# Optimization experiments

Hardware: AMD Instinct MI355X
Metric: run time of the kernel (lower is better)

The kernel has to match this reference:

```python
import jax, jax.numpy as jnp
import numpy as np

NG, NQ, E, H, L, B = 500000, 100000, 1000000, 128, 4, 1024
EMB, GDIM, NTYPES = 16, 32, 31


def _xavier(key, shape):
    fan_in, fan_out = shape[-2], shape[-1]
    lim = float(np.sqrt(6.0 / (fan_in + fan_out)))
    return jax.random.uniform(key, shape, minval=-lim, maxval=lim, dtype=jnp.float32)


def setup_inputs():
    key = jax.random.key(0)
    ks = iter(jax.random.split(key, 64))
    nk = lambda: next(ks)
    inp = {}
    inp["gate_type_idx"] = jax.random.randint(nk(), (NG,), 0, NTYPES)
    inp["gate_arity"] = jax.random.randint(nk(), (NG,), 1, 3)
    inp["gate_is_directional"] = jax.random.randint(nk(), (NG,), 0, 2)
    inp["gate_index_norm"] = jax.random.uniform(nk(), (NG,), dtype=jnp.float32)
    inp["qubit_degree_norm"] = jax.random.uniform(nk(), (NQ,), dtype=jnp.float32)
    inp["src_g2q"] = jax.random.randint(nk(), (E,), 0, NG)
    inp["dst_g2q"] = jax.random.randint(nk(), (E,), 0, NQ)
    inp["src_q2g"] = jax.random.randint(nk(), (E,), 0, NQ)
    inp["dst_q2g"] = jax.random.randint(nk(), (E,), 0, NG)
    inp["gate_batch"] = jnp.sort(jax.random.randint(nk(), (NG,), 0, B))
    inp["qubit_batch"] = jnp.sort(jax.random.randint(nk(), (NQ,), 0, B))
    inp["global_features"] = jax.random.normal(nk(), (B, GDIM), dtype=jnp.float32)
    inp["backend_bit"] = jax.random.randint(nk(), (B,), 0, 2).astype(jnp.float32)
    inp["precision_bit"] = jax.random.randint(nk(), (B,), 0, 2).astype(jnp.float32)
    inp["emb_table"] = jax.random.normal(nk(), (NTYPES, EMB), dtype=jnp.float32) / np.sqrt(EMB).astype(np.float32)
    inp["gate_proj_W"] = _xavier(nk(), (EMB + 3, H)); inp["gate_proj_b"] = jnp.zeros((H,), jnp.float32)
    inp["qubit_proj_W"] = _xavier(nk(), (1, H)); inp["qubit_proj_b"] = jnp.zeros((H,), jnp.float32)
    inp["g2q_ll_W"] = _xavier(nk(), (L, H, H)); inp["g2q_ll_b"] = jnp.zeros((L, H), jnp.float32)
    inp["g2q_lr_W"] = _xavier(nk(), (L, H, H)); inp["g2q_lr_b"] = jnp.zeros((L, H), jnp.float32)
    inp["q2g_ll_W"] = _xavier(nk(), (L, H, H)); inp["q2g_ll_b"] = jnp.zeros((L, H), jnp.float32)
    inp["q2g_lr_W"] = _xavier(nk(), (L, H, H)); inp["q2g_lr_b"] = jnp.zeros((L, H), jnp.float32)
    inp["gate_ln_g"] = jnp.ones((L, H), jnp.float32); inp["gate_ln_b"] = jnp.zeros((L, H), jnp.float32)
    inp["qubit_ln_g"] = jnp.ones((L, H), jnp.float32); inp["qubit_ln_b"] = jnp.zeros((L, H), jnp.float32)
    inp["glob_W"] = _xavier(nk(), (GDIM, H)); inp["glob_b"] = jnp.zeros((H,), jnp.float32)
    inp["backbone_W"] = _xavier(nk(), (5 * H + 2, H)); inp["backbone_b"] = jnp.zeros((H,), jnp.float32)
    inp["thr_W"] = _xavier(nk(), (H, 10)); inp["thr_b"] = jnp.zeros((10,), jnp.float32)
    inp["run_W"] = _xavier(nk(), (H, 1)); inp["run_b"] = jnp.zeros((1,), jnp.float32)
    return inp


def _layernorm(x, g, b, eps=1e-5):
    m = x.mean(-1, keepdims=True)
    v = jnp.mean((x - m) ** 2, axis=-1, keepdims=True)
    return (x - m) * jax.lax.rsqrt(v + eps) * g + b


def _seg_mean(x, idx, n):
    s = jax.ops.segment_sum(x, idx, num_segments=n)
    c = jax.ops.segment_sum(jnp.ones((x.shape[0], 1), x.dtype), idx, num_segments=n)
    return s / jnp.maximum(c, 1.0)


def reference(gate_type_idx, gate_arity, gate_is_directional, gate_index_norm,
              qubit_degree_norm, src_g2q, dst_g2q, src_q2g, dst_q2g,
              gate_batch, qubit_batch, global_features, backend_bit, precision_bit,
              emb_table, gate_proj_W, gate_proj_b, qubit_proj_W, qubit_proj_b,
              g2q_ll_W, g2q_ll_b, g2q_lr_W, g2q_lr_b,
              q2g_ll_W, q2g_ll_b, q2g_lr_W, q2g_lr_b,
              gate_ln_g, gate_ln_b, qubit_ln_g, qubit_ln_b,
              glob_W, glob_b, backbone_W, backbone_b, thr_W, thr_b, run_W, run_b):
    gate_feat = jnp.concatenate([
        emb_table[gate_type_idx],
        gate_arity[:, None].astype(jnp.float32),
        gate_is_directional[:, None].astype(jnp.float32),
        gate_index_norm[:, None]], axis=1)                      # [NG, EMB+3]
    gx = gate_feat @ gate_proj_W + gate_proj_b                  # [NG, H]
    qx = qubit_degree_norm[:, None] @ qubit_proj_W + qubit_proj_b  # [NQ, H]
    for l in range(L):
        # SAGEConv((H,H),H) per edge type: mean-aggregate src msgs, lin_l(agg)+lin_r(x_dst)
        agg_q = _seg_mean(gx[src_g2q], dst_g2q, NQ)
        q_new = agg_q @ g2q_ll_W[l] + g2q_ll_b[l] + qx @ g2q_lr_W[l] + g2q_lr_b[l]
        agg_g = _seg_mean(qx[src_q2g], dst_q2g, NG)
        g_new = agg_g @ q2g_ll_W[l] + q2g_ll_b[l] + gx @ q2g_lr_W[l] + q2g_lr_b[l]
        gx = _layernorm(jax.nn.silu(g_new), gate_ln_g[l], gate_ln_b[l]) + gx
        qx = _layernorm(jax.nn.silu(q_new), qubit_ln_g[l], qubit_ln_b[l]) + qx
    gm = _seg_mean(gx, gate_batch, B)
    gstd = jnp.sqrt(jnp.maximum(_seg_mean(gx * gx, gate_batch, B) - gm * gm, 1e-6))
    qm = _seg_mean(qx, qubit_batch, B)
    qstd = jnp.sqrt(jnp.maximum(_seg_mean(qx * qx, qubit_batch, B) - qm * qm, 1e-6))
    glob = jax.nn.silu(global_features @ glob_W + glob_b)
    combined = jnp.concatenate([gm, gstd, qm, qstd, glob,
                                backend_bit[:, None], precision_bit[:, None]], axis=1)
    feat = jax.nn.silu(combined @ backbone_W + backbone_b)
    threshold_logits = feat @ thr_W + thr_b                     # [B, 10]
    log_runtime = (feat @ run_W + run_b)[:, 0]                  # [B]
    return threshold_logits, log_runtime
```

## Files before the change

### kernel.cpp

```cpp
#include <hip/hip_runtime.h>
#include <hip/hip_bf16.h>


#define NGATE 500000
#define NQUB  100000
#define NEDGE 1000000
#define H     128
#define NL    4
#define NB    1024
#define EMB   16
#define GDIM  32
#define NTYPES 31

typedef unsigned int u32;
typedef unsigned short u16;
typedef __attribute__((ext_vector_type(8))) short short8;
typedef __attribute__((ext_vector_type(4))) float f32x4;

__device__ __forceinline__ float silu_f(float x) { return x / (1.f + __expf(-x)); }
__device__ __forceinline__ u16 f2bf(float f) {
  __hip_bfloat16 h = __float2bfloat16(f);
  u16 r;
  __builtin_memcpy(&r, &h, 2);
  return r;
}
__device__ __forceinline__ u32 pack2(float a, float b) {
  return (u32)f2bf(a) | ((u32)f2bf(b) << 16);
}
__device__ __forceinline__ float2 unpack2(u32 v) {
  return make_float2(__uint_as_float((v & 0xffffu) << 16), __uint_as_float((v >> 16) << 16));
}
__device__ __forceinline__ float bf16tof(u16 h) { return __uint_as_float(((u32)h) << 16); }

__global__ void k_sentinel(float* out) { out[0] = 10000.f; }


__global__ __launch_bounds__(256) void k_gate_proj(
    const int* __restrict__ ty, const int* __restrict__ ar, const int* __restrict__ di,
    const float* __restrict__ ixn, const float* __restrict__ emb,
    const float* __restrict__ W, const float* __restrict__ bias, u32* __restrict__ gx) {
  __shared__ float sW[19 * H];
  __shared__ float se[NTYPES * EMB];
  __shared__ float sb[H];
  for (int i = threadIdx.x; i < 19 * H; i += 256) sW[i] = W[i];
  for (int i = threadIdx.x; i < NTYPES * EMB; i += 256) se[i] = emb[i];
  if (threadIdx.x < H) sb[threadIdx.x] = bias[threadIdx.x];
  __syncthreads();
  const float2* sW2 = (const float2*)sW;
  const float2* sb2 = (const float2*)sb;
  int lane = threadIdx.x & 63, wid = threadIdx.x >> 6;
  int gw = blockIdx.x * 4 + wid, nw = gridDim.x * 4;
  for (int r = gw; r < NGATE; r += nw) {
    int t = ty[r];
    float fa = (float)ar[r], fd = (float)di[r], fi = ixn[r];
    float2 b2v = sb2[lane];
    float al = b2v.x, ah = b2v.y;
#pragma unroll
    for (int k = 0; k < EMB; k++) {
      float e = se[t * EMB + k];
      float2 w = sW2[k * 64 + lane];
      al += e * w.x;
      ah += e * w.y;
    }
    float2 wa = sW2[16 * 64 + lane], wd = sW2[17 * 64 + lane], wi = sW2[18 * 64 + lane];
    al += fa * wa.x + fd * wd.x + fi * wi.x;
    ah += fa * wa.y + fd * wd.y + fi * wi.y;
    gx[(size_t)r * 64 + lane] = pack2(al, ah);
  }
}

__global__ __launch_bounds__(256) void k_qubit_proj(
    const float* __restrict__ deg, const float* __restrict__ W,
    const float* __restrict__ b, u32* __restrict__ qx) {
  int idx = blockIdx.x * 256 + threadIdx.x;
  if (idx >= NQUB * 64) return;
  int r = idx >> 6, l = idx & 63;
  float d = deg[r];
  qx[idx] = pack2(d * W[2 * l] + b[2 * l], d * W[2 * l + 1] + b[2 * l + 1]);
}


__global__ __launch_bounds__(256) void k_count(
    const int* __restrict__ dq, const int* __restrict__ dg,
    int* __restrict__ cq, int* __restrict__ cg) {
  int e = blockIdx.x * 256 + threadIdx.x;
  if (e >= NEDGE) return;
  atomicAdd(&cq[dq[e]], 1);
  atomicAdd(&cg[dg[e]], 1);
}

__global__ __launch_bounds__(1024) void k_scan_chunk(
    const int* __restrict__ cnt, int n, int* __restrict__ out, int* __restrict__ bsum) {
  __shared__ int s[1024];
  int i = blockIdx.x * 1024 + threadIdx.x;
  int v = (i < n) ? cnt[i] : 0;
  s[threadIdx.x] = v;
  __syncthreads();
  for (int d = 1; d < 1024; d <<= 1) {
    int t = (threadIdx.x >= d) ? s[threadIdx.x - d] : 0;
    __syncthreads();
    s[threadIdx.x] += t;
    __syncthreads();
  }
  if (i < n) out[i] = s[threadIdx.x];
  if (threadIdx.x == 1023 && bsum) bsum[blockIdx.x] = s[1023];
}

__global__ __launch_bounds__(1024) void k_scan_add(
    int n, int* __restrict__ off, const int* __restrict__ bscan) {
  int i = blockIdx.x * 1024 + threadIdx.x;
  if (i < n && blockIdx.x > 0) off[i + 1] += bscan[blockIdx.x - 1];
  if (i == 0) off[0] = 0;
}

__global__ __launch_bounds__(256) void k_csr_fill(
    const int* __restrict__ sq, const int* __restrict__ dq,
    const int* __restrict__ sg, const int* __restrict__ dg,
    const int* __restrict__ offq, const int* __restrict__ offg,
    int* __restrict__ fq, int* __restrict__ fg,
    int* __restrict__ csrq, int* __restrict__ csrg) {
  int e = blockIdx.x * 256 + threadIdx.x;
  if (e >= NEDGE) return;
  int d1 = dq[e];
  int p1 = atomicAdd(&fq[d1], 1);
  csrq[offq[d1] + p1] = sq[e];
  int d2 = dg[e];
  int p2 = atomicAdd(&fg[d2], 1);
  csrg[offg[d2] + p2] = sg[e];
}


__global__ __launch_bounds__(256) void k_prep_w(
    const float* __restrict__ g2q_ll, const float* __restrict__ g2q_lr,
    const float* __restrict__ q2g_ll, const float* __restrict__ q2g_lr,
    u16* __restrict__ Whi, u16* __restrict__ Wlo) {
  int t = blockIdx.x * 256 + threadIdx.x;
  if (t >= 8 * 256 * 128) return;
  int o = t & 127, k = (t >> 7) & 255, mat = t >> 15;
  int l = mat >> 1, side = mat & 1;
  const float* Wll = side ? q2g_ll : g2q_ll;
  const float* Wlr = side ? q2g_lr : g2q_lr;
  float w = (k < 128) ? Wll[((size_t)l * 128 + k) * 128 + o]
                      : Wlr[((size_t)l * 128 + (k - 128)) * 128 + o];
  u16 hi = f2bf(w);
  float lof = w - bf16tof(hi);
  int ks = k >> 5, kr = k & 31, ot = o >> 4;
  int lane = ((kr >> 3) << 4) | (o & 15);
  int j = kr & 7;
  size_t pos = (((size_t)(mat * 8 + ks) * 8 + ot) * 64 + lane) * 8 + j;
  Whi[pos] = hi;
  Wlo[pos] = f2bf(lof);
}

__global__ __launch_bounds__(256) void k_prep_b(
    const float* __restrict__ g2q_llb, const float* __restrict__ g2q_lrb,
    const float* __restrict__ q2g_llb, const float* __restrict__ q2g_lrb,
    float* __restrict__ bcat) {
  int t = blockIdx.x * 256 + threadIdx.x;
  if (t >= 8 * 128) return;
  int c = t & 127, mat = t >> 7, l = mat >> 1, side = mat & 1;
  bcat[t] = side ? (q2g_llb[l * 128 + c] + q2g_lrb[l * 128 + c])
                 : (g2q_llb[l * 128 + c] + g2q_lrb[l * 128 + c]);
}


__global__ __launch_bounds__(256) void k_gather_rows(
    const u32* __restrict__ SRC, const int* __restrict__ off, const int* __restrict__ csr,
    u32* __restrict__ OUT, int n) {
  int lane = threadIdx.x & 63, wid = threadIdx.x >> 6;
  int w = blockIdx.x * 4 + wid, nw = gridDim.x * 4;
  for (int r = w; r < n; r += nw) {
    int b = off[r], e = off[r + 1];
    float sl = 0.f, sh = 0.f;
    for (int t = b; t < e; t += 8) {
      u32 v[8];
      float wt_[8];
#pragma unroll
      for (int j = 0; j < 8; j++) {
        int tj = min(t + j, e - 1);
        wt_[j] = (j == 0 || t + j < e) ? 1.f : 0.f;
        v[j] = SRC[(size_t)csr[tj] * 64 + lane];
      }
#pragma unroll
      for (int j = 0; j < 8; j++) {
        float2 f = unpack2(v[j]);
        sl += wt_[j] * f.x;
        sh += wt_[j] * f.y;
      }
    }
    float inv = 1.f / fmaxf((float)(e - b), 1.f);
    OUT[(size_t)r * 64 + lane] = pack2(sl * inv, sh * inv);
  }
}


template <int GATHER>
__global__ __launch_bounds__(256, 2) void k_layer(
    const u16* __restrict__ AGG16, const u16* __restrict__ SRC16,
    const int* __restrict__ off, const int* __restrict__ csr,
    u32* __restrict__ X, const u16* __restrict__ Whi, const u16* __restrict__ Wlo,
    const float* __restrict__ bcat, const float* __restrict__ lng,
    const float* __restrict__ lnb, int nrows) {
  __shared__ __align__(16) float sMemF[4 * 16 * 132];
  u16* sBp = (u16*)sMemF;
  int tid = threadIdx.x;
  int lane = tid & 63, wid = tid >> 6;
  long wt = (long)blockIdx.x * 4 + wid;
  long r0 = wt * 32;
  bool wvalid = (r0 < nrows);
  long r0c = wvalid ? r0 : 0;
  int rlo = lane & 15, khi = lane >> 4;
  u16* X16 = (u16*)X;

  uint4 h0, h1, l0, l1;
#define LOADB(KS) { \
    const uint4* sh_ = (const uint4*)(Whi + (size_t)(KS) * 4096); \
    const uint4* sl_ = (const uint4*)(Wlo + (size_t)(KS) * 4096); \
    h0 = sh_[tid]; h1 = sh_[256 + tid]; l0 = sl_[tid]; l1 = sl_[256 + tid]; }
#define WRITEB(BUF) { \
    ((uint4*)(sBp + (size_t)(BUF) * 8192))[tid] = h0; \
    ((uint4*)(sBp + (size_t)(BUF) * 8192))[256 + tid] = h1; \
    ((uint4*)(sBp + (size_t)(BUF) * 8192 + 4096))[tid] = l0; \
    ((uint4*)(sBp + (size_t)(BUF) * 8192 + 4096))[256 + tid] = l1; }

  LOADB(0);
  WRITEB(0);
  LOADB(1);

  short8 ag[2][4], xg[2][4];
#pragma unroll
  for (int rs = 0; rs < 2; rs++) {
    long row = r0c + rs * 16 + rlo;
#pragma unroll
    for (int ks = 0; ks < 4; ks++)
      xg[rs][ks] = *(const short8*)(X16 + row * 128 + ks * 32 + khi * 8);
    if (GATHER == 0) {
#pragma unroll
      for (int ks = 0; ks < 4; ks++)
        ag[rs][ks] = *(const short8*)(AGG16 + row * 128 + ks * 32 + khi * 8);
    } else {
      int bgn = off[row], end = off[row + 1];
      float m[4][8];
#pragma unroll
      for (int ks = 0; ks < 4; ks++)
#pragma unroll
        for (int j = 0; j < 8; j++) m[ks][j] = 0.f;
      for (int t = bgn; t < end; t += 2) {
        int t1 = min(t + 1, end - 1);
        float w1 = (t + 1 < end) ? 1.f : 0.f;
        const u16* p0 = SRC16 + (size_t)csr[t] * 128 + khi * 8;
        const u16* p1 = SRC16 + (size_t)csr[t1] * 128 + khi * 8;
        uint4 va[4] = {*(const uint4*)(p0), *(const uint4*)(p0 + 32),
                       *(const uint4*)(p0 + 64), *(const uint4*)(p0 + 96)};
        uint4 vb[4] = {*(const uint4*)(p1), *(const uint4*)(p1 + 32),
                       *(const uint4*)(p1 + 64), *(const uint4*)(p1 + 96)};
#pragma unroll
        for (int ks = 0; ks < 4; ks++) {
          m[ks][0] += __uint_as_float((va[ks].x & 0xffffu) << 16) + w1 * __uint_as_float((vb[ks].x & 0xffffu) << 16);
          m[ks][1] += __uint_as_float((va[ks].x >> 16) << 16) + w1 * __uint_as_float((vb[ks].x >> 16) << 16);
          m[ks][2] += __uint_as_float((va[ks].y & 0xffffu) << 16) + w1 * __uint_as_float((vb[ks].y & 0xffffu) << 16);
          m[ks][3] += __uint_as_float((va[ks].y >> 16) << 16) + w1 * __uint_as_float((vb[ks].y >> 16) << 16);
          m[ks][4] += __uint_as_float((va[ks].z & 0xffffu) << 16) + w1 * __uint_as_float((vb[ks].z & 0xffffu) << 16);
          m[ks][5] += __uint_as_float((va[ks].z >> 16) << 16) + w1 * __uint_as_float((vb[ks].z >> 16) << 16);
          m[ks][6] += __uint_as_float((va[ks].w & 0xffffu) << 16) + w1 * __uint_as_float((vb[ks].w & 0xffffu) << 16);
          m[ks][7] += __uint_as_float((va[ks].w >> 16) << 16) + w1 * __uint_as_float((vb[ks].w >> 16) << 16);
        }
      }
      float inv = 1.f / fmaxf((float)(end - bgn), 1.f);
#pragma unroll
      for (int ks = 0; ks < 4; ks++) {
        short8 af;
#pragma unroll
        for (int j = 0; j < 8; j++) af[j] = (short)f2bf(m[ks][j] * inv);
        ag[rs][ks] = af;
      }
    }
  }

  __syncthreads();

  f32x4 acc[2][8];
#pragma unroll
  for (int rs = 0; rs < 2; rs++)
#pragma unroll
    for (int ot = 0; ot < 8; ot++) acc[rs][ot] = (f32x4){0.f, 0.f, 0.f, 0.f};

#pragma unroll
  for (int ks = 0; ks < 8; ks++) {
    const u16* sH = sBp + (size_t)(ks & 1) * 8192;
    const u16* sL = sH + 4096;
    short8 a0 = (ks < 4) ? ag[0][ks & 3] : xg[0][ks & 3];
    short8 a1 = (ks < 4) ? ag[1][ks & 3] : xg[1][ks & 3];
#pragma unroll
    for (int ot = 0; ot < 8; ot++) {
      short8 bh = *(const short8*)(sH + ot * 512 + lane * 8);
      short8 bl = *(const short8*)(sL + ot * 512 + lane * 8);
      acc[0][ot] = __builtin_amdgcn_mfma_f32_16x16x32_bf16(a0, bh, acc[0][ot], 0, 0, 0);
      acc[0][ot] = __builtin_amdgcn_mfma_f32_16x16x32_bf16(a0, bl, acc[0][ot], 0, 0, 0);
      acc[1][ot] = __builtin_amdgcn_mfma_f32_16x16x32_bf16(a1, bh, acc[1][ot], 0, 0, 0);
      acc[1][ot] = __builtin_amdgcn_mfma_f32_16x16x32_bf16(a1, bl, acc[1][ot], 0, 0, 0);
    }
    if (ks < 7) {
      WRITEB((ks + 1) & 1);
      if (ks < 6) LOADB(ks + 2);
      __syncthreads();
    }
  }
#undef LOADB
#undef WRITEB

  __syncthreads();
  if (!wvalid) return;
  float* sE = sMemF + wid * (16 * 132);

  float bz[8], lg[8], lb[8];
#pragma unroll
  for (int ot = 0; ot < 8; ot++) {
    int c = ot * 16 + rlo;
    bz[ot] = bcat[c];
    lg[ot] = lng[c];
    lb[ot] = lnb[c];
  }

#pragma unroll
  for (int rs = 0; rs < 2; rs++) {
#pragma unroll
    for (int ks = 0; ks < 4; ks++) {
      float* p = sE + rlo * 132 + ks * 32 + khi * 8;
      float4 t0, t1;
      t0.x = bf16tof((u16)xg[rs][ks][0]); t0.y = bf16tof((u16)xg[rs][ks][1]);
      t0.z = bf16tof((u16)xg[rs][ks][2]); t0.w = bf16tof((u16)xg[rs][ks][3]);
      t1.x = bf16tof((u16)xg[rs][ks][4]); t1.y = bf16tof((u16)xg[rs][ks][5]);
      t1.z = bf16tof((u16)xg[rs][ks][6]); t1.w = bf16tof((u16)xg[rs][ks][7]);
      *(float4*)p = t0;
      *((float4*)p + 1) = t1;
    }
#pragma unroll
    for (int i = 0; i < 4; i++) {
      long row = r0 + rs * 16 + khi * 4 + i;
      int row_l = khi * 4 + i;
      float u[8], s1 = 0.f, s2 = 0.f;
#pragma unroll
      for (int ot = 0; ot < 8; ot++) {
        float z = acc[rs][ot][i] + bz[ot];
        float uu = silu_f(z);
        u[ot] = uu;
        s1 += uu;
        s2 += uu * uu;
      }
#pragma unroll
      for (int msk = 1; msk < 16; msk <<= 1) {
        s1 += __shfl_xor(s1, msk, 64);
        s2 += __shfl_xor(s2, msk, 64);
      }
      float mean = s1 * (1.f / 128.f);
      float var = s2 * (1.f / 128.f) - mean * mean;
      float rsq = rsqrtf(var + 1e-5f);
#pragma unroll
      for (int ot = 0; ot < 8; ot++) {
        float xr = sE[row_l * 132 + ot * 16 + rlo];
        float o = (u[ot] - mean) * rsq * lg[ot] + lb[ot] + xr;
        X16[(size_t)row * 128 + ot * 16 + rlo] = f2bf(o);
      }
    }
  }
}


__global__ __launch_bounds__(256) void k_seg_counts(
    const int* __restrict__ batch, float* __restrict__ bcnt, int n) {
  int t = blockIdx.x * 256 + threadIdx.x;
  int r0 = t * 64;
  if (r0 >= n) return;
  int end = min(r0 + 64, n);
  int cur = batch[r0];
  float c = 0.f;
  for (int r = r0; r < end; r++) {
    int b = batch[r];
    if (b != cur) { atomicAdd(&bcnt[cur], c); cur = b; c = 0.f; }
    c += 1.f;
  }
  atomicAdd(&bcnt[cur], c);
}

__global__ __launch_bounds__(256) void k_bstats(
    const u32* __restrict__ X, const int* __restrict__ batch,
    float* __restrict__ bsum, float* __restrict__ bsq, int nrows) {
  __shared__ int sb[64];
  int R0 = blockIdx.x * 64;
  int tid = threadIdx.x, lane = tid & 63, wid = tid >> 6;
  if (tid < 64) sb[tid] = (R0 + tid < nrows) ? batch[R0 + tid] : -1;
  __syncthreads();
  int rbase = wid * 16;
  if (R0 + rbase >= nrows) return;
  int c0 = 2 * lane, c1 = 2 * lane + 1;
  float s0 = 0.f, s1 = 0.f, q0 = 0.f, q1 = 0.f;
  int cur = sb[rbase];
  for (int i = 0; i < 16; i++) {
    int r = R0 + rbase + i;
    if (r >= nrows) break;
    int b = sb[rbase + i];
    if (b != cur) {
      atomicAdd(&bsum[cur * H + c0], s0);
      atomicAdd(&bsum[cur * H + c1], s1);
      atomicAdd(&bsq[cur * H + c0], q0);
      atomicAdd(&bsq[cur * H + c1], q1);
      s0 = s1 = q0 = q1 = 0.f;
      cur = b;
    }
    float2 v = unpack2(X[(size_t)r * 64 + lane]);
    s0 += v.x; s1 += v.y;
    q0 += v.x * v.x; q1 += v.y * v.y;
  }
  atomicAdd(&bsum[cur * H + c0], s0);
  atomicAdd(&bsum[cur * H + c1], s1);
  atomicAdd(&bsq[cur * H + c0], q0);
  atomicAdd(&bsq[cur * H + c1], q1);
}

__global__ __launch_bounds__(128) void k_head(
    const float* __restrict__ bsum_g, const float* __restrict__ bsq_g, const float* __restrict__ bcnt_g,
    const float* __restrict__ bsum_q, const float* __restrict__ bsq_q, const float* __restrict__ bcnt_q,
    const float* __restrict__ gf, const float* __restrict__ backend, const float* __restrict__ precision,
    const float* __restrict__ globW, const float* __restrict__ globb,
    const float* __restrict__ bbW, const float* __restrict__ bbb,
    const float* __restrict__ thrW, const float* __restrict__ thrb,
    const float* __restrict__ runW, const float* __restrict__ runb,
    float* __restrict__ out) {
  __shared__ float comb[5 * H + 2];
  __shared__ float feat[H];
  int b = blockIdx.x, c = threadIdx.x;
  float ig = 1.f / fmaxf(bcnt_g[b], 1.f);
  float iq = 1.f / fmaxf(bcnt_q[b], 1.f);
  float gm = bsum_g[b * H + c] * ig;
  float gs = sqrtf(fmaxf(bsq_g[b * H + c] * ig - gm * gm, 1e-6f));
  float qm = bsum_q[b * H + c] * iq;
  float qs = sqrtf(fmaxf(bsq_q[b * H + c] * iq - qm * qm, 1e-6f));
  float gl = globb[c];
#pragma unroll
  for (int j = 0; j < GDIM; j++) gl += gf[b * GDIM + j] * globW[j * H + c];
  gl = silu_f(gl);
  comb[c] = gm;
  comb[H + c] = gs;
  comb[2 * H + c] = qm;
  comb[3 * H + c] = qs;
  comb[4 * H + c] = gl;
  if (c == 0) {
    comb[5 * H] = backend[b];
    comb[5 * H + 1] = precision[b];
  }
  __syncthreads();
  float f = bbb[c];
  for (int k = 0; k < 5 * H + 2; k++) f += comb[k] * bbW[k * H + c];
  f = silu_f(f);
  feat[c] = f;
  __syncthreads();
  if (c < 10) {
    float o = thrb[c];
#pragma unroll
    for (int k = 0; k < H; k++) o += feat[k] * thrW[k * 10 + c];
    out[b * 10 + c] = o;
  }
  if (c == 64) {
    float o = runb[0];
    for (int k = 0; k < H; k++) o += feat[k] * runW[k];
    out[NB * 10 + b] = o;
  }
}


extern "C" void kernel_launch(void* const* d_in, const int* in_sizes, int n_in,
                              void* d_out, int out_size, void* d_ws, size_t ws_size,
                              hipStream_t stream) {
  const int* gate_type = (const int*)d_in[0];
  const int* gate_arity = (const int*)d_in[1];
  const int* gate_dir = (const int*)d_in[2];
  const float* gate_ixn = (const float*)d_in[3];
  const float* qdeg = (const float*)d_in[4];
  const int* src_g2q = (const int*)d_in[5];
  const int* dst_g2q = (const int*)d_in[6];
  const int* src_q2g = (const int*)d_in[7];
  const int* dst_q2g = (const int*)d_in[8];
  const int* gate_batch = (const int*)d_in[9];
  const int* qubit_batch = (const int*)d_in[10];
  const float* gfeat = (const float*)d_in[11];
  const float* backend = (const float*)d_in[12];
  const float* precision = (const float*)d_in[13];
  const float* emb = (const float*)d_in[14];
  const float* gpW = (const float*)d_in[15];
  const float* gpb = (const float*)d_in[16];
  const float* qpW = (const float*)d_in[17];
  const float* qpb = (const float*)d_in[18];
  const float* g2q_ll_W = (const float*)d_in[19];
  const float* g2q_ll_b = (const float*)d_in[20];
  const float* g2q_lr_W = (const float*)d_in[21];
  const float* g2q_lr_b = (const float*)d_in[22];
  const float* q2g_ll_W = (const float*)d_in[23];
  const float* q2g_ll_b = (const float*)d_in[24];
  const float* q2g_lr_W = (const float*)d_in[25];
  const float* q2g_lr_b = (const float*)d_in[26];
  const float* gate_ln_g = (const float*)d_in[27];
  const float* gate_ln_b = (const float*)d_in[28];
  const float* qubit_ln_g = (const float*)d_in[29];
  const float* qubit_ln_b = (const float*)d_in[30];
  const float* globW = (const float*)d_in[31];
  const float* globb = (const float*)d_in[32];
  const float* bbW = (const float*)d_in[33];
  const float* bbb = (const float*)d_in[34];
  const float* thrW = (const float*)d_in[35];
  const float* thrb = (const float*)d_in[36];
  const float* runW = (const float*)d_in[37];
  const float* runb = (const float*)d_in[38];

  char* base = (char*)d_ws;
  u32* gx    = (u32*)base;
  u32* qx    = gx + (size_t)NGATE * 64;
  u32* agg_q = qx + (size_t)NQUB * 64;
  u16* Whi   = (u16*)(agg_q + (size_t)NQUB * 64);
  u16* Wlo   = Whi + 8 * 32768;
  float* bcat = (float*)(Wlo + 8 * 32768);
  int* offq = (int*)(bcat + 8 * 128);
  int* offg = offq + (NQUB + 1);
  int* csrq = offg + (NGATE + 1);
  int* csrg = csrq + NEDGE;
  int* cntq = csrg + NEDGE;
  int* cntg = cntq + NQUB;
  int* bsumA = cntg + NGATE;
  int* bsumB = bsumA + 512;
  float* bsum_g = (float*)(bsumB + 512);
  float* bsq_g  = bsum_g + NB * H;
  float* bsum_q = bsq_g + NB * H;
  float* bsq_q  = bsum_q + NB * H;
  float* bcnt_g = bsq_q + NB * H;
  float* bcnt_q = bcnt_g + NB;
  size_t need = (size_t)((char*)(bcnt_q + NB) - base);
  if (ws_size < need) {
    k_sentinel<<<1, 1, 0, stream>>>((float*)d_out);
    return;
  }

  k_prep_w<<<(8 * 256 * 128 + 255) / 256, 256, 0, stream>>>(
      g2q_ll_W, g2q_lr_W, q2g_ll_W, q2g_lr_W, Whi, Wlo);
  k_prep_b<<<4, 256, 0, stream>>>(g2q_ll_b, g2q_lr_b, q2g_ll_b, q2g_lr_b, bcat);

  hipMemsetAsync(cntq, 0, (size_t)(NQUB + NGATE) * sizeof(int), stream);
  k_count<<<(NEDGE + 255) / 256, 256, 0, stream>>>(dst_g2q, dst_q2g, cntq, cntg);
  const int nbq = (NQUB + 1023) / 1024, nbg = (NGATE + 1023) / 1024;
  k_scan_chunk<<<nbq, 1024, 0, stream>>>(cntq, NQUB, offq + 1, bsumA);
  k_scan_chunk<<<1, 1024, 0, stream>>>(bsumA, nbq, bsumB, nullptr);
  k_scan_add<<<nbq, 1024, 0, stream>>>(NQUB, offq, bsumB);
  k_scan_chunk<<<nbg, 1024, 0, stream>>>(cntg, NGATE, offg + 1, bsumA);
  k_scan_chunk<<<1, 1024, 0, stream>>>(bsumA, nbg, bsumB, nullptr);
  k_scan_add<<<nbg, 1024, 0, stream>>>(NGATE, offg, bsumB);
  hipMemsetAsync(cntq, 0, (size_t)(NQUB + NGATE) * sizeof(int), stream);
  k_csr_fill<<<(NEDGE + 255) / 256, 256, 0, stream>>>(
      src_g2q, dst_g2q, src_q2g, dst_q2g, offq, offg, cntq, cntg, csrq, csrg);

  size_t stats_floats = 4ULL * NB * H + 2ULL * NB;
  hipMemsetAsync(bsum_g, 0, stats_floats * sizeof(float), stream);
  k_seg_counts<<<(NGATE / 64 + 256) / 256, 256, 0, stream>>>(gate_batch, bcnt_g, NGATE);
  k_seg_counts<<<(NQUB / 64 + 256) / 256, 256, 0, stream>>>(qubit_batch, bcnt_q, NQUB);

  k_gate_proj<<<1024, 256, 0, stream>>>(gate_type, gate_arity, gate_dir, gate_ixn,
                                        emb, gpW, gpb, gx);
  k_qubit_proj<<<(NQUB * 64 + 255) / 256, 256, 0, stream>>>(qdeg, qpW, qpb, qx);

  const int blocks_g = (NGATE + 127) / 128;
  const int blocks_q = (NQUB + 127) / 128;
  for (int l = 0; l < NL; l++) {
    const u16* WhiG = Whi + (size_t)(l * 2 + 1) * 32768;
    const u16* WloG = Wlo + (size_t)(l * 2 + 1) * 32768;
    const float* bcG = bcat + (l * 2 + 1) * 128;
    const u16* WhiQ = Whi + (size_t)(l * 2) * 32768;
    const u16* WloQ = Wlo + (size_t)(l * 2) * 32768;
    const float* bcQ = bcat + (l * 2) * 128;
    k_gather_rows<<<(NQUB + 3) / 4, 256, 0, stream>>>(gx, offq, csrq, agg_q, NQUB);
    k_layer<1><<<blocks_g, 256, 0, stream>>>(
        nullptr, (const u16*)qx, offg, csrg, gx,
        WhiG, WloG, bcG, gate_ln_g + (size_t)l * H, gate_ln_b + (size_t)l * H, NGATE);
    k_layer<0><<<blocks_q, 256, 0, stream>>>(
        (const u16*)agg_q, nullptr, nullptr, nullptr, qx,
        WhiQ, WloQ, bcQ, qubit_ln_g + (size_t)l * H, qubit_ln_b + (size_t)l * H, NQUB);
  }

  k_bstats<<<(NGATE + 63) / 64, 256, 0, stream>>>(gx, gate_batch, bsum_g, bsq_g, NGATE);
  k_bstats<<<(NQUB + 63) / 64, 256, 0, stream>>>(qx, qubit_batch, bsum_q, bsq_q, NQUB);
  k_head<<<NB, 128, 0, stream>>>(bsum_g, bsq_g, bcnt_g, bsum_q, bsq_q, bcnt_q,
                                 gfeat, backend, precision, globW, globb,
                                 bbW, bbb, thrW, thrb, runW, runb, (float*)d_out);
}
```

Before: 1.351 ms.

## Fuse qubit gather into layer kernel and snapshot qx for gate update

Drops the separate k_gather_rows kernel and the agg_q intermediate. The qubit layer kernel now does its own CSR mean-gather from gx, with a 4-way unrolled edge loop, and runs before the gate layer. Because the qubit update now overwrites qx before the gate layer reads it, qx is first copied to a snapshot buffer, and the gate layer gathers from that copy with a 2-way unroll. This removes one launch and the write and read of the aggregate buffer, at the cost of a 25.6 MB device-to-device copy per layer and gather latency now inside the qubit MFMA kernel.

```diff
diff --git a/kernel.cpp b/kernel.cpp
--- a/kernel.cpp
+++ b/kernel.cpp
@@ -164,39 +164,9 @@
 }
 
 
-__global__ __launch_bounds__(256) void k_gather_rows(
-    const u32* __restrict__ SRC, const int* __restrict__ off, const int* __restrict__ csr,
-    u32* __restrict__ OUT, int n) {
-  int lane = threadIdx.x & 63, wid = threadIdx.x >> 6;
-  int w = blockIdx.x * 4 + wid, nw = gridDim.x * 4;
-  for (int r = w; r < n; r += nw) {
-    int b = off[r], e = off[r + 1];
-    float sl = 0.f, sh = 0.f;
-    for (int t = b; t < e; t += 8) {
-      u32 v[8];
-      float wt_[8];
-#pragma unroll
-      for (int j = 0; j < 8; j++) {
-        int tj = min(t + j, e - 1);
-        wt_[j] = (j == 0 || t + j < e) ? 1.f : 0.f;
-        v[j] = SRC[(size_t)csr[tj] * 64 + lane];
-      }
-#pragma unroll
-      for (int j = 0; j < 8; j++) {
-        float2 f = unpack2(v[j]);
-        sl += wt_[j] * f.x;
-        sh += wt_[j] * f.y;
-      }
-    }
-    float inv = 1.f / fmaxf((float)(e - b), 1.f);
-    OUT[(size_t)r * 64 + lane] = pack2(sl * inv, sh * inv);
-  }
-}
-
-
-template <int GATHER>
+template <int U>
 __global__ __launch_bounds__(256, 2) void k_layer(
-    const u16* __restrict__ AGG16, const u16* __restrict__ SRC16,
+    const u16* __restrict__ SRC16,
     const int* __restrict__ off, const int* __restrict__ csr,
     u32* __restrict__ X, const u16* __restrict__ Whi, const u16* __restrict__ Wlo,
     const float* __restrict__ bcat, const float* __restrict__ lng,
@@ -234,46 +204,47 @@
 #pragma unroll
     for (int ks = 0; ks < 4; ks++)
       xg[rs][ks] = *(const short8*)(X16 + row * 128 + ks * 32 + khi * 8);
-    if (GATHER == 0) {
-#pragma unroll
-      for (int ks = 0; ks < 4; ks++)
-        ag[rs][ks] = *(const short8*)(AGG16 + row * 128 + ks * 32 + khi * 8);
-    } else {
-      int bgn = off[row], end = off[row + 1];
-      float m[4][8];
-#pragma unroll
-      for (int ks = 0; ks < 4; ks++)
-#pragma unroll
-        for (int j = 0; j < 8; j++) m[ks][j] = 0.f;
-      for (int t = bgn; t < end; t += 2) {
-        int t1 = min(t + 1, end - 1);
-        float w1 = (t + 1 < end) ? 1.f : 0.f;
-        const u16* p0 = SRC16 + (size_t)csr[t] * 128 + khi * 8;
-        const u16* p1 = SRC16 + (size_t)csr[t1] * 128 + khi * 8;
-        uint4 va[4] = {*(const uint4*)(p0), *(const uint4*)(p0 + 32),
-                       *(const uint4*)(p0 + 64), *(const uint4*)(p0 + 96)};
-        uint4 vb[4] = {*(const uint4*)(p1), *(const uint4*)(p1 + 32),
-                       *(const uint4*)(p1 + 64), *(const uint4*)(p1 + 96)};
+    int bgn = off[row], end = off[row + 1];
+    float m[4][8];
+#pragma unroll
+    for (int ks = 0; ks < 4; ks++)
+#pragma unroll
+      for (int j = 0; j < 8; j++) m[ks][j] = 0.f;
+    for (int t = bgn; t < end; t += U) {
+      uint4 v[U][4];
+      float w_[U];
+#pragma unroll
+      for (int u = 0; u < U; u++) {
+        int tu = min(t + u, end - 1);
+        w_[u] = (u == 0 || t + u < end) ? 1.f : 0.f;
+        const u16* p = SRC16 + (size_t)csr[tu] * 128 + khi * 8;
+        v[u][0] = *(const uint4*)(p);
+        v[u][1] = *(const uint4*)(p + 32);
+        v[u][2] = *(const uint4*)(p + 64);
+        v[u][3] = *(const uint4*)(p + 96);
+      }
+#pragma unroll
+      for (int u = 0; u < U; u++) {
 #pragma unroll
         for (int ks = 0; ks < 4; ks++) {
-          m[ks][0] += __uint_as_float((va[ks].x & 0xffffu) << 16) + w1 * __uint_as_float((vb[ks].x & 0xffffu) << 16);
-          m[ks][1] += __uint_as_float((va[ks].x >> 16) << 16) + w1 * __uint_as_float((vb[ks].x >> 16) << 16);
-          m[ks][2] += __uint_as_float((va[ks].y & 0xffffu) << 16) + w1 * __uint_as_float((vb[ks].y & 0xffffu) << 16);
-          m[ks][3] += __uint_as_float((va[ks].y >> 16) << 16) + w1 * __uint_as_float((vb[ks].y >> 16) << 16);
-          m[ks][4] += __uint_as_float((va[ks].z & 0xffffu) << 16) + w1 * __uint_as_float((vb[ks].z & 0xffffu) << 16);
-          m[ks][5] += __uint_as_float((va[ks].z >> 16) << 16) + w1 * __uint_as_float((vb[ks].z >> 16) << 16);
-          m[ks][6] += __uint_as_float((va[ks].w & 0xffffu) << 16) + w1 * __uint_as_float((vb[ks].w & 0xffffu) << 16);
-          m[ks][7] += __uint_as_float((va[ks].w >> 16) << 16) + w1 * __uint_as_float((vb[ks].w >> 16) << 16);
+          m[ks][0] += w_[u] * __uint_as_float((v[u][ks].x & 0xffffu) << 16);
+          m[ks][1] += w_[u] * __uint_as_float((v[u][ks].x >> 16) << 16);
+          m[ks][2] += w_[u] * __uint_as_float((v[u][ks].y & 0xffffu) << 16);
+          m[ks][3] += w_[u] * __uint_as_float((v[u][ks].y >> 16) << 16);
+          m[ks][4] += w_[u] * __uint_as_float((v[u][ks].z & 0xffffu) << 16);
+          m[ks][5] += w_[u] * __uint_as_float((v[u][ks].z >> 16) << 16);
+          m[ks][6] += w_[u] * __uint_as_float((v[u][ks].w & 0xffffu) << 16);
+          m[ks][7] += w_[u] * __uint_as_float((v[u][ks].w >> 16) << 16);
         }
       }
-      float inv = 1.f / fmaxf((float)(end - bgn), 1.f);
-#pragma unroll
-      for (int ks = 0; ks < 4; ks++) {
-        short8 af;
-#pragma unroll
-        for (int j = 0; j < 8; j++) af[j] = (short)f2bf(m[ks][j] * inv);
-        ag[rs][ks] = af;
-      }
+    }
+    float inv = 1.f / fmaxf((float)(end - bgn), 1.f);
+#pragma unroll
+    for (int ks = 0; ks < 4; ks++) {
+      short8 af;
+#pragma unroll
+      for (int j = 0; j < 8; j++) af[j] = (short)f2bf(m[ks][j] * inv);
+      ag[rs][ks] = af;
     }
   }
 
@@ -515,8 +486,8 @@
   char* base = (char*)d_ws;
   u32* gx    = (u32*)base;
   u32* qx    = gx + (size_t)NGATE * 64;
-  u32* agg_q = qx + (size_t)NQUB * 64;
-  u16* Whi   = (u16*)(agg_q + (size_t)NQUB * 64);
+  u32* qx_old= qx + (size_t)NQUB * 64;
+  u16* Whi   = (u16*)(qx_old + (size_t)NQUB * 64);
   u16* Wlo   = Whi + 8 * 32768;
   float* bcat = (float*)(Wlo + 8 * 32768);
   int* offq = (int*)(bcat + 8 * 128);
@@ -574,13 +545,14 @@
     const u16* WhiQ = Whi + (size_t)(l * 2) * 32768;
     const u16* WloQ = Wlo + (size_t)(l * 2) * 32768;
     const float* bcQ = bcat + (l * 2) * 128;
-    k_gather_rows<<<(NQUB + 3) / 4, 256, 0, stream>>>(gx, offq, csrq, agg_q, NQUB);
-    k_layer<1><<<blocks_g, 256, 0, stream>>>(
-        nullptr, (const u16*)qx, offg, csrg, gx,
+    hipMemcpyAsync(qx_old, qx, (size_t)NQUB * 64 * sizeof(u32),
+                   hipMemcpyDeviceToDevice, stream);
+    k_layer<4><<<blocks_q, 256, 0, stream>>>(
+        (const u16*)gx, offq, csrq, qx,
+        WhiQ, WloQ, bcQ, qubit_ln_g + (size_t)l * H, qubit_ln_b + (size_t)l * H, NQUB);
+    k_layer<2><<<blocks_g, 256, 0, stream>>>(
+        (const u16*)qx_old, offg, csrg, gx,
         WhiG, WloG, bcG, gate_ln_g + (size_t)l * H, gate_ln_b + (size_t)l * H, NGATE);
-    k_layer<0><<<blocks_q, 256, 0, stream>>>(
-        (const u16*)agg_q, nullptr, nullptr, nullptr, qx,
-        WhiQ, WloQ, bcQ, qubit_ln_g + (size_t)l * H, qubit_ln_b + (size_t)l * H, NQUB);
   }
 
   k_bstats<<<(NGATE + 63) / 64, 256, 0, stream>>>(gx, gate_batch, bsum_g, bsq_g, NGATE);
```

New measurement: 1.500 ms. 11.0% more time.
